# Performance work log

Hardware: AMD Instinct MI355X
Metric: run time of the kernel (lower is better)

Reference implementation:

```python
import jax, jax.numpy as jnp
import numpy as np

TEMPERATURE = 0.7
BIG_NEG = -1e30  # safe stand-in for -inf (keeps grads finite)


def setup_inputs() -> dict:
    key = jax.random.key(0)
    k1, k2, k3 = jax.random.split(key, 3)
    B, D = 8192, 256
    embeddings = jax.random.normal(k1, (B, D), dtype=jnp.float32)
    categories = jax.random.randint(k2, (B,), 0, 16, dtype=jnp.int64)
    font_labels = jax.random.randint(k3, (B,), 0, 2000, dtype=jnp.int64)
    return {"embeddings": embeddings, "categories": categories, "font_labels": font_labels}


def reference(embeddings, categories, font_labels):
    # L2-normalize rows
    e = embeddings / jnp.linalg.norm(embeddings, axis=1, keepdims=True)
    sims = jnp.matmul(e, e.T) / TEMPERATURE  # [B, B]
    B = sims.shape[0]

    same = categories[:, None] == categories[None, :]
    diag = jnp.eye(B, dtype=bool)
    pos_mask = same & ~diag           # same category, excluding self
    neg_mask = ~same                  # different category (self excluded implicitly)

    valid = pos_mask.any(axis=1) & neg_mask.any(axis=1)

    pos_sim = jnp.max(jnp.where(pos_mask, sims, BIG_NEG), axis=1)  # hardest positive per anchor
    neg_max = jnp.max(jnp.where(neg_mask, sims, BIG_NEG), axis=1)

    # logsumexp over {pos_sim} U neg_sims, numerically stable
    m = jnp.where(valid, jnp.maximum(pos_sim, neg_max), 0.0)
    pos_safe = jnp.where(valid, pos_sim, 0.0)
    exp_neg_sum = jnp.sum(jnp.where(neg_mask, jnp.exp(sims - m[:, None]), 0.0), axis=1)
    lse = m + jnp.log(jnp.exp(pos_safe - m) + exp_neg_sum)

    loss_per_anchor = -pos_safe + lse
    n_valid = jnp.maximum(jnp.sum(valid), 1)
    return jnp.sum(jnp.where(valid, loss_per_anchor, 0.0)) / n_valid
```

## Files before the change

### kernel.cpp

```cpp
#include <hip/hip_runtime.h>
#include <stdint.h>

#define NROWS 8192
#define DDIM 256
#define NSTRIPS 32
#define STRIP_COLS 256
#define BN 32
#define NTILES 8
#define BM 128
#define NSLOT NSTRIPS

#define ESCALE 1.4356159f
#define LN2F   0.6931471806f
#define NEGBIG (-1e30f)

typedef __attribute__((ext_vector_type(8))) short short8;
typedef __attribute__((ext_vector_type(4))) float f32x4;

__device__ __forceinline__ unsigned short f2bf(float x) {
  unsigned int u = __float_as_uint(x);
  u += 0x7fffu + ((u >> 16) & 1u);
  return (unsigned short)(u >> 16);
}

__global__ __launch_bounds__(256) void knorm(const float* __restrict__ emb,
                                             unsigned short* __restrict__ ebfB,
                                             uint4* __restrict__ accv) {
  if (blockIdx.x == 0 && threadIdx.x == 0) *accv = (uint4){0u, 0u, 0u, 0u};
  const int wave = threadIdx.x >> 6, lane = threadIdx.x & 63;
  const int row = blockIdx.x * 4 + wave;
  const float4 v = *(const float4*)(emb + row * DDIM + lane * 4);
  float ss = v.x * v.x + v.y * v.y + v.z * v.z + v.w * v.w;
#pragma unroll
  for (int off = 1; off < 64; off <<= 1) ss += __shfl_xor(ss, off, 64);
  const float sc = rsqrtf(ss) * ESCALE;
  ushort4 o;
  o.x = f2bf(v.x * sc); o.y = f2bf(v.y * sc);
  o.z = f2bf(v.z * sc); o.w = f2bf(v.w * sc);
  *(ushort4*)(ebfB + ((lane >> 1) * NROWS + row) * 8 + (lane & 1) * 4) = o;
}

__global__ __launch_bounds__(256) void kmain(const unsigned short* __restrict__ ebfB,
                                             const int* __restrict__ cats,
                                             float* __restrict__ posP,
                                             float* __restrict__ sumP) {
  const int tid = threadIdx.x;
  const int lane = tid & 63;
  const int lane15 = lane & 15, quad = lane >> 4;
  const int wave = tid >> 6;
  const int strip = blockIdx.x, rowTile = blockIdx.y;
  const int rowG = rowTile * BM + wave * 32;
  const int col0 = strip * STRIP_COLS;

  short8 a[2][8];
#pragma unroll
  for (int m = 0; m < 2; ++m)
#pragma unroll
    for (int kk = 0; kk < 8; ++kk)
      a[m][kk] = *(const short8*)(ebfB +
          ((size_t)(kk * 4 + quad) * NROWS + rowG + m * 16 + lane15) * 8);

  int cati[2][4];
#pragma unroll
  for (int m = 0; m < 2; ++m)
#pragma unroll
    for (int r = 0; r < 4; ++r)
      cati[m][r] = cats[rowG + m * 16 + quad * 4 + r];

  bool dlr[4];
#pragma unroll
  for (int r = 0; r < 4; ++r) dlr[r] = (lane15 == quad * 4 + r);

  float pm[2][4], ns[2][4];
#pragma unroll
  for (int m = 0; m < 2; ++m)
#pragma unroll
    for (int r = 0; r < 4; ++r) { pm[m][r] = NEGBIG; ns[m][r] = 0.f; }

  const unsigned short* bbase = ebfB + ((size_t)quad * NROWS + col0 + lane15) * 8;

#define LOADB(buf, t, nt)                                                       \
  _Pragma("unroll")                                                             \
  for (int kk = 0; kk < 8; ++kk)                                                \
    buf[kk] = *(const short8*)(bbase +                                          \
        ((size_t)kk * 4 * NROWS + (t) * BN + (nt) * 16) * 8);

#define DOMFMA(buf, ACC0, ACC1)                                                 \
  f32x4 ACC0 = {0.f, 0.f, 0.f, 0.f}, ACC1 = {0.f, 0.f, 0.f, 0.f};              \
  _Pragma("unroll")                                                             \
  for (int kk = 0; kk < 8; ++kk) {                                              \
    ACC0 = __builtin_amdgcn_mfma_f32_16x16x32_bf16(a[0][kk], buf[kk], ACC0, 0, 0, 0); \
    ACC1 = __builtin_amdgcn_mfma_f32_16x16x32_bf16(a[1][kk], buf[kk], ACC1, 0, 0, 0); \
  }

#define EPI(ACC0, ACC1, t, nt)                                                  \
  {                                                                             \
    const int colBase = col0 + (t) * BN + (nt) * 16;                            \
    const int cj = cats[colBase + lane15];                                      \
    const bool dg0 = (rowG == colBase);                                         \
    const bool dg1 = (rowG + 16 == colBase);                                    \
    _Pragma("unroll")                                                           \
    for (int m = 0; m < 2; ++m) {                                               \
      const bool dg = m ? dg1 : dg0;                                            \
      _Pragma("unroll")                                                         \
      for (int r = 0; r < 4; ++r) {                                             \
        const float s = m ? ACC1[r] : ACC0[r];         \
        const float e = __builtin_amdgcn_exp2f(s);                              \
        const bool same = (cj == cati[m][r]);                                   \
        float psv = same ? s : NEGBIG;                                          \
        if (dg) psv = dlr[r] ? NEGBIG : psv;           \
        pm[m][r] = fmaxf(pm[m][r], psv);                                        \
        ns[m][r] += same ? 0.f : e;                                             \
      }                                                                         \
    }                                                                           \
  }

  short8 b0[8], b1[8];
  LOADB(b0, 0, 0);

  for (int t = 0; t < NTILES; ++t) {
    LOADB(b1, t, 1);
    { DOMFMA(b0, acc0, acc1) EPI(acc0, acc1, t, 0) }
    if (t + 1 < NTILES) LOADB(b0, t + 1, 0);
    { DOMFMA(b1, acc2, acc3) EPI(acc2, acc3, t, 1) }
  }

#pragma unroll
  for (int off = 1; off < 16; off <<= 1) {
#pragma unroll
    for (int m = 0; m < 2; ++m)
#pragma unroll
      for (int r = 0; r < 4; ++r) {
        pm[m][r] = fmaxf(pm[m][r], __shfl_xor(pm[m][r], off, 64));
        ns[m][r] += __shfl_xor(ns[m][r], off, 64);
      }
  }
  if (lane15 == 0) {
#pragma unroll
    for (int m = 0; m < 2; ++m)
#pragma unroll
      for (int r = 0; r < 4; ++r) {
        const int row = rowG + m * 16 + quad * 4 + r;
        posP[strip * NROWS + row] = pm[m][r];
        sumP[strip * NROWS + row] = ns[m][r];
      }
  }
}

__global__ __launch_bounds__(256) void kmerge(const float* __restrict__ posP,
                                              const float* __restrict__ sumP,
                                              float* __restrict__ acc,
                                              float* __restrict__ out) {
  const int row = blockIdx.x * 256 + threadIdx.x;
  float pm = NEGBIG, ns = 0.f;
#pragma unroll 8
  for (int s = 0; s < NSLOT; ++s) {
    pm = fmaxf(pm, posP[s * NROWS + row]);
    ns += sumP[s * NROWS + row];
  }
  const bool valid = (pm > -1e29f) && (ns > 0.f);
  float loss = valid ? (logf(__builtin_amdgcn_exp2f(pm) + ns) - pm * LN2F) : 0.f;
  float cnt = valid ? 1.f : 0.f;
#pragma unroll
  for (int off = 1; off < 64; off <<= 1) {
    loss += __shfl_xor(loss, off, 64);
    cnt += __shfl_xor(cnt, off, 64);
  }
  if ((threadIdx.x & 63) == 0) {
    atomicAdd(&acc[0], loss);
    atomicAdd(&acc[1], cnt);
    __threadfence();
  }
  __syncthreads();
  if (threadIdx.x == 0) {
    const int prev = atomicAdd((int*)(acc + 2), 1);
    if (prev == (int)gridDim.x - 1) {
      const float L = atomicAdd(&acc[0], 0.f);
      const float C = atomicAdd(&acc[1], 0.f);
      out[0] = L / fmaxf(C, 1.f);
    }
  }
}

extern "C" void kernel_launch(void* const* d_in, const int* in_sizes, int n_in,
                              void* d_out, int out_size, void* d_ws, size_t ws_size,
                              hipStream_t stream) {
  const float* emb = (const float*)d_in[0];
  const int* cats = (const int*)d_in[1];
  float* out = (float*)d_out;

  char* ws = (char*)d_ws;
  float* accv = (float*)ws;
  unsigned short* ebfB = (unsigned short*)(ws + 256);
  float* posP = (float*)(ws + 256 + (size_t)NROWS * DDIM * 2);
  float* sumP = posP + NSLOT * NROWS;

  knorm<<<NROWS / 4, 256, 0, stream>>>(emb, ebfB, (uint4*)ws);
  kmain<<<dim3(NSTRIPS, NROWS / BM), 256, 0, stream>>>(ebfB, cats, posP, sumP);
  kmerge<<<NROWS / 256, 256, 0, stream>>>(posP, sumP, accv, out);
}
```

Measured before the change: 114.8 us.

## Exploit symmetry of similarity matrix to compute only upper-triangular tiles

Since the similarity matrix is symmetric, each block now handles only the row tiles at or above the diagonal within its column strip. While computing its own rows it also reduces column-wise partial max and exp-sums, which stand in for the mirrored rows. This roughly halves the MFMA and exp work. In exchange it adds a triangular block index decode, shared-memory column reductions, more partial slots (96 instead of 32) with order-preserving integer keys for the max, and zeroing of the whole partial buffer in knorm, so kmerge reads three times as much data.

```diff
diff --git a/kernel.cpp b/kernel.cpp
--- a/kernel.cpp
+++ b/kernel.cpp
@@ -3,16 +3,22 @@
 
 #define NROWS 8192
 #define DDIM 256
-#define NSTRIPS 32
+#define NJ2 32
 #define STRIP_COLS 256
 #define BN 32
 #define NTILES 8
 #define BM 128
-#define NSLOT NSTRIPS
+#define NBLK 1056
+#define NSLOT 96
 
 #define ESCALE 1.4356159f
 #define LN2F   0.6931471806f
 #define NEGBIG (-1e30f)
+
+#define WS_PMK   256
+#define WS_NS    (WS_PMK + NSLOT * NROWS * 4)
+#define WS_EBF   (WS_NS + NSLOT * NROWS * 4)
+#define WS_ZERO16 ((WS_EBF) / 16)
 
 typedef __attribute__((ext_vector_type(8))) short short8;
 typedef __attribute__((ext_vector_type(4))) float f32x4;
@@ -23,10 +29,20 @@
   return (unsigned short)(u >> 16);
 }
 
+__device__ __forceinline__ unsigned fkey(float f) {
+  unsigned b = __float_as_uint(f);
+  return (b & 0x80000000u) ? ~b : (b | 0x80000000u);
+}
+__device__ __forceinline__ float funkey(unsigned k) {
+  unsigned b = (k & 0x80000000u) ? (k & 0x7fffffffu) : ~k;
+  return __uint_as_float(b);
+}
+
 __global__ __launch_bounds__(256) void knorm(const float* __restrict__ emb,
                                              unsigned short* __restrict__ ebfB,
-                                             uint4* __restrict__ accv) {
-  if (blockIdx.x == 0 && threadIdx.x == 0) *accv = (uint4){0u, 0u, 0u, 0u};
+                                             uint4* __restrict__ zbase) {
+  const int zi = blockIdx.x * 256 + threadIdx.x;
+  if (zi < WS_ZERO16) zbase[zi] = (uint4){0u, 0u, 0u, 0u};
   const int wave = threadIdx.x >> 6, lane = threadIdx.x & 63;
   const int row = blockIdx.x * 4 + wave;
   const float4 v = *(const float4*)(emb + row * DDIM + lane * 4);
@@ -42,15 +58,20 @@
 
 __global__ __launch_bounds__(256) void kmain(const unsigned short* __restrict__ ebfB,
                                              const int* __restrict__ cats,
-                                             float* __restrict__ posP,
+                                             unsigned* __restrict__ posPk,
                                              float* __restrict__ sumP) {
+  int bid = blockIdx.x, I = 0, base = 0;
+  for (;; ++I) { const int c = NJ2 - (I >> 1); if (bid < base + c) break; base += c; }
+  const int J2 = (I >> 1) + (bid - base);
+  const int col0 = J2 * STRIP_COLS;
+  const int t0 = (I * BM > col0) ? (NTILES / 2) : 0;
+
+  __shared__ float cpmL[4][STRIP_COLS], cnsL[4][STRIP_COLS];
   const int tid = threadIdx.x;
   const int lane = tid & 63;
   const int lane15 = lane & 15, quad = lane >> 4;
   const int wave = tid >> 6;
-  const int strip = blockIdx.x, rowTile = blockIdx.y;
-  const int rowG = rowTile * BM + wave * 32;
-  const int col0 = strip * STRIP_COLS;
+  const int rowG = I * BM + wave * 32;
 
   short8 a[2][8];
 #pragma unroll
@@ -99,6 +120,7 @@
     const int cj = cats[colBase + lane15];                                      \
     const bool dg0 = (rowG == colBase);                                         \
     const bool dg1 = (rowG + 16 == colBase);                                    \
+    float cpmv = NEGBIG, cnsv = 0.f;                                            \
     _Pragma("unroll")                                                           \
     for (int m = 0; m < 2; ++m) {                                               \
       const bool dg = m ? dg1 : dg0;                                            \
@@ -110,15 +132,26 @@
         float psv = same ? s : NEGBIG;                                          \
         if (dg) psv = dlr[r] ? NEGBIG : psv;           \
         pm[m][r] = fmaxf(pm[m][r], psv);                                        \
-        ns[m][r] += same ? 0.f : e;                                             \
+        const float ev = same ? 0.f : e;                                        \
+        ns[m][r] += ev;                                                         \
+        cpmv = fmaxf(cpmv, psv);                                                \
+        cnsv += ev;                                                             \
       }                                                                         \
     }                                                                           \
+    if ((colBase >> 7) > I) {                \
+      cpmv = fmaxf(cpmv, __shfl_xor(cpmv, 16, 64)); cnsv += __shfl_xor(cnsv, 16, 64); \
+      cpmv = fmaxf(cpmv, __shfl_xor(cpmv, 32, 64)); cnsv += __shfl_xor(cnsv, 32, 64); \
+      if (quad == 0) {                                                          \
+        cpmL[wave][(t) * BN + (nt) * 16 + lane15] = cpmv;                       \
+        cnsL[wave][(t) * BN + (nt) * 16 + lane15] = cnsv;                       \
+      }                                                                         \
+    }                                                                           \
   }
 
   short8 b0[8], b1[8];
-  LOADB(b0, 0, 0);
-
-  for (int t = 0; t < NTILES; ++t) {
+  LOADB(b0, t0, 0);
+
+  for (int t = t0; t < NTILES; ++t) {
     LOADB(b1, t, 1);
     { DOMFMA(b0, acc0, acc1) EPI(acc0, acc1, t, 0) }
     if (t + 1 < NTILES) LOADB(b0, t + 1, 0);
@@ -141,23 +174,35 @@
 #pragma unroll
       for (int r = 0; r < 4; ++r) {
         const int row = rowG + m * 16 + quad * 4 + r;
-        posP[strip * NROWS + row] = pm[m][r];
-        sumP[strip * NROWS + row] = ns[m][r];
+        posPk[J2 * NROWS + row] = fkey(pm[m][r]);
+        sumP [J2 * NROWS + row] = ns[m][r];
       }
   }
-}
-
-__global__ __launch_bounds__(256) void kmerge(const float* __restrict__ posP,
+
+  __syncthreads();
+  const int cs = (I + 1) * BM - col0;
+  const int c = tid;
+  if (c >= cs) {
+    const float p = fmaxf(fmaxf(cpmL[0][c], cpmL[1][c]),
+                          fmaxf(cpmL[2][c], cpmL[3][c]));
+    const float n = cnsL[0][c] + cnsL[1][c] + cnsL[2][c] + cnsL[3][c];
+    posPk[(NJ2 + I) * NROWS + col0 + c] = fkey(p);
+    sumP [(NJ2 + I) * NROWS + col0 + c] = n;
+  }
+}
+
+__global__ __launch_bounds__(256) void kmerge(const unsigned* __restrict__ posPk,
                                               const float* __restrict__ sumP,
                                               float* __restrict__ acc,
                                               float* __restrict__ out) {
   const int row = blockIdx.x * 256 + threadIdx.x;
-  float pm = NEGBIG, ns = 0.f;
+  unsigned kmax = 0u; float ns = 0.f;
 #pragma unroll 8
   for (int s = 0; s < NSLOT; ++s) {
-    pm = fmaxf(pm, posP[s * NROWS + row]);
+    kmax = max(kmax, posPk[s * NROWS + row]);
     ns += sumP[s * NROWS + row];
   }
+  const float pm = funkey(kmax);
   const bool valid = (pm > -1e29f) && (ns > 0.f);
   float loss = valid ? (logf(__builtin_amdgcn_exp2f(pm) + ns) - pm * LN2F) : 0.f;
   float cnt = valid ? 1.f : 0.f;
@@ -191,11 +236,11 @@
 
   char* ws = (char*)d_ws;
   float* accv = (float*)ws;
-  unsigned short* ebfB = (unsigned short*)(ws + 256);
-  float* posP = (float*)(ws + 256 + (size_t)NROWS * DDIM * 2);
-  float* sumP = posP + NSLOT * NROWS;
+  unsigned* posPk = (unsigned*)(ws + WS_PMK);
+  float* sumP = (float*)(ws + WS_NS);
+  unsigned short* ebfB = (unsigned short*)(ws + WS_EBF);
 
   knorm<<<NROWS / 4, 256, 0, stream>>>(emb, ebfB, (uint4*)ws);
-  kmain<<<dim3(NSTRIPS, NROWS / BM), 256, 0, stream>>>(ebfB, cats, posP, sumP);
-  kmerge<<<NROWS / 256, 256, 0, stream>>>(posP, sumP, accv, out);
-}
+  kmain<<<NBLK, 256, 0, stream>>>(ebfB, cats, posPk, sumP);
+  kmerge<<<NROWS / 256, 256, 0, stream>>>(posPk, sumP, accv, out);
+}
```

Result: no change. 116.7 us (+1.6%).
